# Performance work log

Measured on AMD Instinct MI355X. Metric: run time of the kernel, lower is better.

Reference implementation:

```python
import jax, jax.numpy as jnp
import numpy as np

B, NL, NP, E = 64, 128, 128, 4096


def setup_inputs() -> dict:
    key = jax.random.key(0)
    k1, k2, k3, k4, k5 = jax.random.split(key, 5)
    P = jax.random.uniform(k1, (B, NL, NP), dtype=jnp.float32)
    # normalize rows so P looks like soft assignment probabilities
    P = P / P.sum(-1, keepdims=True)
    d_error = jax.random.uniform(k2, (NP, NP), dtype=jnp.float32)
    edge_weights = jax.random.uniform(k3, (B, E), dtype=jnp.float32)
    d_hw = jax.random.randint(k4, (NP, NP), 0, 6, dtype=jnp.int32)
    edge_pairs = jax.random.randint(k5, (B, E, 2), 0, NL, dtype=jnp.int64)
    return {"P": P, "d_error": d_error, "edge_weights": edge_weights,
            "d_hw": d_hw, "edge_pairs": edge_pairs}


def reference(P, d_error, edge_weights, d_hw, edge_pairs):
    # A_fidelity = adjacency (d_hw == 1) weighted by clamped fidelity
    A_fid = (d_hw == 1).astype(P.dtype) * jnp.maximum(1.0 - d_error, 0.0)  # [Np,Np]
    i = edge_pairs[..., 0]  # [B,E]
    j = edge_pairs[..., 1]  # [B,E]
    Pi = jnp.take_along_axis(P, i[..., None], axis=1)  # [B,E,Np] gather of P[b,i,:]
    Pj = jnpp = jnp.take_along_axis(P, j[..., None], axis=1)  # [B,E,Np]
    # per-edge score: P[b,i,:] @ A_fid @ P[b,j,:]
    scores = jnp.einsum('bep,pq,beq->be', Pi, A_fid, Pj)
    w_sum = jnp.maximum(edge_weights.sum(-1), 1e-8)  # [B]
    sample_adj = (edge_weights * scores).sum(-1) / w_sum  # [B]
    # all samples have edges -> valid_samples == B
    loss = -sample_adj.mean()
    return loss
```

## Files before the change

kernel.cpp:

```cpp
#include <hip/hip_runtime.h>
#include <hip/hip_bf16.h>

#define B_   64
#define NL_  128
#define NP_  128
#define E_   4096


__global__ __launch_bounds__(256) void k_qgemm(
    const float* __restrict__ P,
    const float* __restrict__ d_error,
    const int*   __restrict__ d_hw,
    float* __restrict__ Q)
{
    __shared__ float As[NP_ * NP_];
    const int t = threadIdx.x;

    const float4* de4 = (const float4*)d_error;
    const int4*   dh4 = (const int4*)d_hw;
    float4* As4 = (float4*)As;
    #pragma unroll
    for (int k = 0; k < 16; ++k) {
        int f = k*256 + t;
        float4 e = de4[f];
        int4   h = dh4[f];
        float4 a;
        a.x = (h.x == 1) ? fmaxf(1.0f - e.x, 0.0f) : 0.0f;
        a.y = (h.y == 1) ? fmaxf(1.0f - e.y, 0.0f) : 0.0f;
        a.z = (h.z == 1) ? fmaxf(1.0f - e.z, 0.0f) : 0.0f;
        a.w = (h.w == 1) ? fmaxf(1.0f - e.w, 0.0f) : 0.0f;
        As4[f] = a;
    }
    __syncthreads();

    const int row0 = blockIdx.x * 16;
    const int tc = t & 31;
    const int tr = t >> 5;
    const float* Pr0 = P + (row0 + 2*tr + 0) * NP_;
    const float* Pr1 = P + (row0 + 2*tr + 1) * NP_;

    float4 acc0 = {0,0,0,0}, acc1 = {0,0,0,0};
    const float4* As4r = (const float4*)As;
    #pragma unroll 8
    for (int p = 0; p < NP_; ++p) {
        float4 av = As4r[p*32 + tc];
        float pv0 = Pr0[p];
        float pv1 = Pr1[p];
        acc0.x = fmaf(pv0, av.x, acc0.x); acc0.y = fmaf(pv0, av.y, acc0.y);
        acc0.z = fmaf(pv0, av.z, acc0.z); acc0.w = fmaf(pv0, av.w, acc0.w);
        acc1.x = fmaf(pv1, av.x, acc1.x); acc1.y = fmaf(pv1, av.y, acc1.y);
        acc1.z = fmaf(pv1, av.z, acc1.z); acc1.w = fmaf(pv1, av.w, acc1.w);
    }
    float4* Q4 = (float4*)(Q + row0 * NP_);
    Q4[(2*tr+0)*32 + tc] = acc0;
    Q4[(2*tr+1)*32 + tc] = acc1;
}

__global__ __launch_bounds__(256) void k_edges(
    const float* __restrict__ P,
    const float* __restrict__ Q,
    const float* __restrict__ ew,
    const int*   __restrict__ pairs_raw,
    float* __restrict__ num_part,
    float* __restrict__ den_part)
{
    const int b     = blockIdx.x >> 3;
    const int chunk = blockIdx.x & 7;
    const int t = threadIdx.x;
    const int g = t >> 5;
    const int c = t & 31;

    int hw = pairs_raw[2*(t & 63) + 1];
    unsigned long long nz = __ballot(hw != 0);
    const int is64 = (nz == 0ULL);

    const float4* Q4 = (const float4*)(Q + (size_t)b * NL_ * NP_);
    const float4* P4 = (const float4*)(P + (size_t)b * NL_ * NP_);
    const float*  wrow = ew + b * E_;

    float acc  = 0.0f;
    float wacc = 0.0f;
    const int ebase = chunk * 512;
    #pragma unroll 8
    for (int k = 0; k < 64; ++k) {
        int e = ebase + k*8 + g;
        long pe = (long)b * E_ + e;
        int i, j;
        if (is64) { i = pairs_raw[4*pe];  j = pairs_raw[4*pe + 2]; }
        else      { i = pairs_raw[2*pe];  j = pairs_raw[2*pe + 1]; }
        float w = wrow[e];
        float4 qv = Q4[i*32 + c];
        float4 pv = P4[j*32 + c];
        acc = fmaf(w, qv.x*pv.x + qv.y*pv.y + qv.z*pv.z + qv.w*pv.w, acc);
        if (c == 0) wacc += w;
    }
    #pragma unroll
    for (int off = 32; off >= 1; off >>= 1) {
        acc  += __shfl_xor(acc,  off, 64);
        wacc += __shfl_xor(wacc, off, 64);
    }
    __shared__ float rs[8];
    const int wid  = t >> 6;
    const int lane = t & 63;
    if (lane == 0) { rs[wid] = acc; rs[4 + wid] = wacc; }
    __syncthreads();
    if (t == 0) {
        num_part[blockIdx.x] = rs[0] + rs[1] + rs[2] + rs[3];
        den_part[blockIdx.x] = rs[4] + rs[5] + rs[6] + rs[7];
    }
}

__global__ __launch_bounds__(64) void k_final(
    const float* __restrict__ num_part,
    const float* __restrict__ den_part,
    float* __restrict__ out)
{
    int b = threadIdx.x;
    float n = 0.0f, d = 0.0f;
    #pragma unroll
    for (int c = 0; c < 8; ++c) {
        n += num_part[b*8 + c];
        d += den_part[b*8 + c];
    }
    float v = n / fmaxf(d, 1e-8f);
    #pragma unroll
    for (int off = 32; off >= 1; off >>= 1) v += __shfl_xor(v, off, 64);
    if (b == 0) out[0] = -v / (float)B_;
}

extern "C" void kernel_launch(void* const* d_in, const int* in_sizes, int n_in,
                              void* d_out, int out_size, void* d_ws, size_t ws_size,
                              hipStream_t stream) {
    const float* P       = (const float*)d_in[0];
    const float* d_error = (const float*)d_in[1];
    const float* ew      = (const float*)d_in[2];
    const int*   d_hw    = (const int*)d_in[3];
    const int*   pairs   = (const int*)d_in[4];
    float* out = (float*)d_out;

    char*  ws  = (char*)d_ws;
    float* Q   = (float*)ws;
    float* num = (float*)(ws + 4194304);
    float* den = (float*)(ws + 4194304 + 2048);

    k_qgemm<<<512, 256, 0, stream>>>(P, d_error, d_hw, Q);
    k_edges<<<512, 256, 0, stream>>>(P, Q, ew, pairs, num, den);
    k_final<<<1,   64,  0, stream>>>(num, den, out);
}
```

Measured before the change: 99.92 us.

## Scatter edge weights into a dense matrix and contract as GEMMs

Instead of gathering Q and P rows for every edge, each block scatters its edge weights with LDS atomics into a dense weight matrix W[j, i] for a 16-row slice of i. It then computes Q = P·A for those rows and R = W^T·P from a full per-sample P tile held in LDS, and reduces Q·R. A small prep kernel builds the masked A matrix once and sums the edge weights per sample. This replaces irregular per-edge global gathers and the large Q intermediate with dense, LDS-resident compute. In exchange every block now reads all of its sample's edges and 64KB of P into LDS, which may cut occupancy and adds atomic contention.

Measured after the change: 96.99 us. -2.9%, faster.

```diff
diff --git a/kernel.cpp b/kernel.cpp
--- a/kernel.cpp
+++ b/kernel.cpp
@@ -7,122 +7,142 @@
 #define E_   4096
 
 
-__global__ __launch_bounds__(256) void k_qgemm(
-    const float* __restrict__ P,
+__global__ __launch_bounds__(256) void k_prep(
     const float* __restrict__ d_error,
     const int*   __restrict__ d_hw,
-    float* __restrict__ Q)
+    const float* __restrict__ ew,
+    float* __restrict__ A,
+    float* __restrict__ den)
 {
-    __shared__ float As[NP_ * NP_];
+    const int b = blockIdx.x;
     const int t = threadIdx.x;
 
-    const float4* de4 = (const float4*)d_error;
-    const int4*   dh4 = (const int4*)d_hw;
-    float4* As4 = (float4*)As;
+    int idx = b * 256 + t;
+    float a = 0.0f;
+    if (d_hw[idx] == 1) a = fmaxf(1.0f - d_error[idx], 0.0f);
+    A[idx] = a;
+
+    const float4* ew4 = (const float4*)(ew + b * E_);
+    float s = 0.0f;
+    #pragma unroll
+    for (int k = 0; k < 4; ++k) {
+        float4 v = ew4[k * 256 + t];
+        s += v.x + v.y + v.z + v.w;
+    }
+    #pragma unroll
+    for (int off = 32; off >= 1; off >>= 1) s += __shfl_xor(s, off, 64);
+    __shared__ float rs[4];
+    if ((t & 63) == 0) rs[t >> 6] = s;
+    __syncthreads();
+    if (t == 0) den[b] = rs[0] + rs[1] + rs[2] + rs[3];
+}
+
+__global__ __launch_bounds__(256) void k_main(
+    const float* __restrict__ P,
+    const float* __restrict__ A,
+    const float* __restrict__ ew,
+    const int*   __restrict__ pairs_raw,
+    float* __restrict__ num_part)
+{
+    __shared__ float Plds[NL_ * NP_];
+    __shared__ float WT[NL_ * 16];
+    __shared__ float red[4];
+
+    const int b     = blockIdx.x >> 3;
+    const int chunk = blockIdx.x & 7;
+    const int r0    = chunk * 16;
+    const int t  = threadIdx.x;
+    const int tr = t >> 5;
+    const int tc = t & 31;
+
+    float4* WT4 = (float4*)WT;
+    WT4[2*t]     = float4{0,0,0,0};
+    WT4[2*t + 1] = float4{0,0,0,0};
+
+    const float4* Pg4 = (const float4*)(P + (size_t)b * NL_ * NP_);
+    float4* Pl4 = (float4*)Plds;
     #pragma unroll
     for (int k = 0; k < 16; ++k) {
-        int f = k*256 + t;
-        float4 e = de4[f];
-        int4   h = dh4[f];
-        float4 a;
-        a.x = (h.x == 1) ? fmaxf(1.0f - e.x, 0.0f) : 0.0f;
-        a.y = (h.y == 1) ? fmaxf(1.0f - e.y, 0.0f) : 0.0f;
-        a.z = (h.z == 1) ? fmaxf(1.0f - e.z, 0.0f) : 0.0f;
-        a.w = (h.w == 1) ? fmaxf(1.0f - e.w, 0.0f) : 0.0f;
-        As4[f] = a;
+        int f = k * 256 + t;
+        Pl4[f] = Pg4[f];
     }
     __syncthreads();
 
-    const int row0 = blockIdx.x * 16;
-    const int tc = t & 31;
-    const int tr = t >> 5;
-    const float* Pr0 = P + (row0 + 2*tr + 0) * NP_;
-    const float* Pr1 = P + (row0 + 2*tr + 1) * NP_;
-
-    float4 acc0 = {0,0,0,0}, acc1 = {0,0,0,0};
-    const float4* As4r = (const float4*)As;
-    #pragma unroll 8
-    for (int p = 0; p < NP_; ++p) {
-        float4 av = As4r[p*32 + tc];
-        float pv0 = Pr0[p];
-        float pv1 = Pr1[p];
-        acc0.x = fmaf(pv0, av.x, acc0.x); acc0.y = fmaf(pv0, av.y, acc0.y);
-        acc0.z = fmaf(pv0, av.z, acc0.z); acc0.w = fmaf(pv0, av.w, acc0.w);
-        acc1.x = fmaf(pv1, av.x, acc1.x); acc1.y = fmaf(pv1, av.y, acc1.y);
-        acc1.z = fmaf(pv1, av.z, acc1.z); acc1.w = fmaf(pv1, av.w, acc1.w);
-    }
-    float4* Q4 = (float4*)(Q + row0 * NP_);
-    Q4[(2*tr+0)*32 + tc] = acc0;
-    Q4[(2*tr+1)*32 + tc] = acc1;
-}
-
-__global__ __launch_bounds__(256) void k_edges(
-    const float* __restrict__ P,
-    const float* __restrict__ Q,
-    const float* __restrict__ ew,
-    const int*   __restrict__ pairs_raw,
-    float* __restrict__ num_part,
-    float* __restrict__ den_part)
-{
-    const int b     = blockIdx.x >> 3;
-    const int chunk = blockIdx.x & 7;
-    const int t = threadIdx.x;
-    const int g = t >> 5;
-    const int c = t & 31;
-
-    int hw = pairs_raw[2*(t & 63) + 1];
+    int hw = pairs_raw[2 * (t & 63) + 1];
     unsigned long long nz = __ballot(hw != 0);
     const int is64 = (nz == 0ULL);
 
-    const float4* Q4 = (const float4*)(Q + (size_t)b * NL_ * NP_);
-    const float4* P4 = (const float4*)(P + (size_t)b * NL_ * NP_);
-    const float*  wrow = ew + b * E_;
+    const float* wrow = ew + (size_t)b * E_;
+    if (is64) {
+        const int4* pp = (const int4*)pairs_raw + (size_t)b * E_;
+        #pragma unroll 4
+        for (int k = 0; k < 16; ++k) {
+            int e = k * 256 + t;
+            int4 pr = pp[e];
+            int i = pr.x, j = pr.z;
+            if (i >= r0 && i < r0 + 16)
+                atomicAdd(&WT[j * 16 + (i - r0)], wrow[e]);
+        }
+    } else {
+        const int2* pp = (const int2*)pairs_raw + (size_t)b * E_;
+        #pragma unroll 4
+        for (int k = 0; k < 16; ++k) {
+            int e = k * 256 + t;
+            int2 pr = pp[e];
+            int i = pr.x, j = pr.y;
+            if (i >= r0 && i < r0 + 16)
+                atomicAdd(&WT[j * 16 + (i - r0)], wrow[e]);
+        }
+    }
 
-    float acc  = 0.0f;
-    float wacc = 0.0f;
-    const int ebase = chunk * 512;
+    const float* Pr0 = P + ((size_t)b * NL_ + r0 + 2*tr) * NP_;
+    const float* Pr1 = Pr0 + NP_;
+    const float4* A4 = (const float4*)A;
+    float4 q0 = {0,0,0,0}, q1 = {0,0,0,0};
     #pragma unroll 8
-    for (int k = 0; k < 64; ++k) {
-        int e = ebase + k*8 + g;
-        long pe = (long)b * E_ + e;
-        int i, j;
-        if (is64) { i = pairs_raw[4*pe];  j = pairs_raw[4*pe + 2]; }
-        else      { i = pairs_raw[2*pe];  j = pairs_raw[2*pe + 1]; }
-        float w = wrow[e];
-        float4 qv = Q4[i*32 + c];
-        float4 pv = P4[j*32 + c];
-        acc = fmaf(w, qv.x*pv.x + qv.y*pv.y + qv.z*pv.z + qv.w*pv.w, acc);
-        if (c == 0) wacc += w;
+    for (int p = 0; p < NP_; ++p) {
+        float4 av = A4[p * 32 + tc];
+        float pv0 = Pr0[p];
+        float pv1 = Pr1[p];
+        q0.x = fmaf(pv0, av.x, q0.x); q0.y = fmaf(pv0, av.y, q0.y);
+        q0.z = fmaf(pv0, av.z, q0.z); q0.w = fmaf(pv0, av.w, q0.w);
+        q1.x = fmaf(pv1, av.x, q1.x); q1.y = fmaf(pv1, av.y, q1.y);
+        q1.z = fmaf(pv1, av.z, q1.z); q1.w = fmaf(pv1, av.w, q1.w);
     }
+    __syncthreads();
+
+    float4 racc0 = {0,0,0,0}, racc1 = {0,0,0,0};
+    const float2* WT2 = (const float2*)WT;
+    const float4* Pl4r = (const float4*)Plds;
+    #pragma unroll 8
+    for (int lp = 0; lp < NL_; ++lp) {
+        float2 w01 = WT2[lp * 8 + tr];
+        float4 pv  = Pl4r[lp * 32 + tc];
+        racc0.x = fmaf(w01.x, pv.x, racc0.x); racc0.y = fmaf(w01.x, pv.y, racc0.y);
+        racc0.z = fmaf(w01.x, pv.z, racc0.z); racc0.w = fmaf(w01.x, pv.w, racc0.w);
+        racc1.x = fmaf(w01.y, pv.x, racc1.x); racc1.y = fmaf(w01.y, pv.y, racc1.y);
+        racc1.z = fmaf(w01.y, pv.z, racc1.z); racc1.w = fmaf(w01.y, pv.w, racc1.w);
+    }
+
+    float nacc = q0.x*racc0.x + q0.y*racc0.y + q0.z*racc0.z + q0.w*racc0.w
+               + q1.x*racc1.x + q1.y*racc1.y + q1.z*racc1.z + q1.w*racc1.w;
     #pragma unroll
-    for (int off = 32; off >= 1; off >>= 1) {
-        acc  += __shfl_xor(acc,  off, 64);
-        wacc += __shfl_xor(wacc, off, 64);
-    }
-    __shared__ float rs[8];
-    const int wid  = t >> 6;
-    const int lane = t & 63;
-    if (lane == 0) { rs[wid] = acc; rs[4 + wid] = wacc; }
+    for (int off = 32; off >= 1; off >>= 1) nacc += __shfl_xor(nacc, off, 64);
+    if ((t & 63) == 0) red[t >> 6] = nacc;
     __syncthreads();
-    if (t == 0) {
-        num_part[blockIdx.x] = rs[0] + rs[1] + rs[2] + rs[3];
-        den_part[blockIdx.x] = rs[4] + rs[5] + rs[6] + rs[7];
-    }
+    if (t == 0) num_part[blockIdx.x] = red[0] + red[1] + red[2] + red[3];
 }
 
 __global__ __launch_bounds__(64) void k_final(
     const float* __restrict__ num_part,
-    const float* __restrict__ den_part,
+    const float* __restrict__ den,
     float* __restrict__ out)
 {
     int b = threadIdx.x;
-    float n = 0.0f, d = 0.0f;
+    float n = 0.0f;
     #pragma unroll
-    for (int c = 0; c < 8; ++c) {
-        n += num_part[b*8 + c];
-        d += den_part[b*8 + c];
-    }
-    float v = n / fmaxf(d, 1e-8f);
+    for (int c = 0; c < 8; ++c) n += num_part[b * 8 + c];
+    float v = n / fmaxf(den[b], 1e-8f);
     #pragma unroll
     for (int off = 32; off >= 1; off >>= 1) v += __shfl_xor(v, off, 64);
     if (b == 0) out[0] = -v / (float)B_;
@@ -139,11 +159,11 @@
     float* out = (float*)d_out;
 
     char*  ws  = (char*)d_ws;
-    float* Q   = (float*)ws;
-    float* num = (float*)(ws + 4194304);
-    float* den = (float*)(ws + 4194304 + 2048);
+    float* A   = (float*)ws;
+    float* num = (float*)(ws + 65536);
+    float* den = (float*)(ws + 65536 + 2048);
 
-    k_qgemm<<<512, 256, 0, stream>>>(P, d_error, d_hw, Q);
-    k_edges<<<512, 256, 0, stream>>>(P, Q, ew, pairs, num, den);
+    k_prep <<<64,  256, 0, stream>>>(d_error, d_hw, ew, A, den);
+    k_main <<<512, 256, 0, stream>>>(P, A, ew, pairs, num);
     k_final<<<1,   64,  0, stream>>>(num, den, out);
 }
```
